# Optimization experiments

Measured on AMD Instinct MI355X. Metric: run time of the kernel, lower is better.

## Reference

```python
import jax, jax.numpy as jnp
import numpy as np

HIDDEN_DIM = 64
MEMORY_SLOTS = 4
SEQ_LEN = 24
VOCAB_SIZE = 64
B = 65536


def setup_inputs() -> dict:
    key = jax.random.key(0)
    ks = jax.random.split(key, 16)
    s = 0.05
    inp = {
        "seqs": jax.random.randint(ks[0], (B, SEQ_LEN), 0, VOCAB_SIZE + 2),
        "query_tok": jax.random.randint(ks[1], (B,), 0, VOCAB_SIZE + 2),
        # embedding table [VOCAB+2, H]
        "embed": jax.random.normal(ks[2], (VOCAB_SIZE + 2, HIDDEN_DIM), jnp.float32) * s,
        # joint_net: Linear(H + S*H -> H), ReLU, Linear(H -> H), ReLU  (weights stored [in, out])
        "W1": jax.random.normal(ks[3], (HIDDEN_DIM + MEMORY_SLOTS * HIDDEN_DIM, HIDDEN_DIM), jnp.float32) * s,
        "b1": jax.random.normal(ks[4], (HIDDEN_DIM,), jnp.float32) * s,
        "W2": jax.random.normal(ks[5], (HIDDEN_DIM, HIDDEN_DIM), jnp.float32) * s,
        "b2": jax.random.normal(ks[6], (HIDDEN_DIM,), jnp.float32) * s,
        # write_head: Linear(H -> H)
        "Ww": jax.random.normal(ks[7], (HIDDEN_DIM, HIDDEN_DIM), jnp.float32) * s,
        "bw": jax.random.normal(ks[8], (HIDDEN_DIM,), jnp.float32) * s,
        # evict_head: Linear(H -> MEMORY_SLOTS)
        "We": jax.random.normal(ks[9], (HIDDEN_DIM, MEMORY_SLOTS), jnp.float32) * s,
        "be": jax.random.normal(ks[10], (MEMORY_SLOTS,), jnp.float32) * s,
        # read_head: Linear(2H -> H), ReLU, Linear(H -> VOCAB)
        "Wr1": jax.random.normal(ks[11], (2 * HIDDEN_DIM, HIDDEN_DIM), jnp.float32) * s,
        "br1": jax.random.normal(ks[12], (HIDDEN_DIM,), jnp.float32) * s,
        "Wr2": jax.random.normal(ks[13], (HIDDEN_DIM, VOCAB_SIZE), jnp.float32) * s,
        "br2": jax.random.normal(ks[14], (VOCAB_SIZE,), jnp.float32) * s,
    }
    return inp


def reference(seqs, query_tok, embed, W1, b1, W2, b2, Ww, bw, We, be, Wr1, br1, Wr2, br2):
    # Token embeddings for the first SEQ_LEN-1 positions, scanned over time: [T, B, H]
    emb_seq = jnp.swapaxes(embed[seqs[:, : SEQ_LEN - 1]], 0, 1)

    def step(mem, emb_t):  # mem: [B, S, H], emb_t: [B, H]
        joint_in = jnp.concatenate([emb_t, mem.reshape(mem.shape[0], -1)], axis=-1)  # [B, H + S*H]
        h = jax.nn.relu(joint_in @ W1 + b1)
        h = jax.nn.relu(h @ W2 + b2)                      # [B, H]
        write_vec = h @ Ww + bw                           # [B, H]
        evict_logits = h @ We + be                        # [B, S]
        evict_idx = jnp.argmax(evict_logits, axis=-1)     # [B] hard, non-diff
        mask = jax.nn.one_hot(evict_idx, MEMORY_SLOTS, dtype=bool)[..., None]  # [B, S, 1]
        new_mem = jnp.where(mask, write_vec[:, None, :], mem)
        return new_mem, None

    mem0 = jnp.zeros((seqs.shape[0], MEMORY_SLOTS, HIDDEN_DIM), jnp.float32)
    mem, _ = jax.lax.scan(step, mem0, emb_seq)

    mem_summary = mem.mean(axis=1)                        # [B, H]
    q_emb = embed[query_tok]                              # [B, H]
    r = jnp.concatenate([q_emb, mem_summary], axis=-1)    # [B, 2H]
    logits = jax.nn.relu(r @ Wr1 + br1) @ Wr2 + br2       # [B, VOCAB]
    return logits
```

## Files before the change

### kernel.cpp

```cpp
#include <hip/hip_runtime.h>

#define H       64
#define NSLOT   4
#define NSTEP   23
#define NB      65536
#define NV      66
#define SEQL    24
#define LPE     8
#define GELEM   2
#define TPB     512
#define EPB     128
#define ACTSTR  132
#define W1RSTR  68
#define W1SSTR  (64 * W1RSTR + 8)

#define OFF_EW1   0
#define OFF_EWR1  (NV * H)

__global__ __launch_bounds__(256) void k_setup_tables(
    const float* __restrict__ embed, const float* __restrict__ W1, const float* __restrict__ b1,
    const float* __restrict__ Wr1, const float* __restrict__ br1, float* __restrict__ ws)
{
    int idx = blockIdx.x * 256 + threadIdx.x;
    if (idx >= NV * H) return;
    int t = idx >> 6, k = idx & 63;
    float a1 = b1[k], a2 = br1[k];
    for (int j = 0; j < H; ++j) {
        float e = embed[t * H + j];
        a1 = fmaf(e, W1[j * H + k], a1);
        a2 = fmaf(e, Wr1[j * H + k], a2);
    }
    ws[OFF_EW1 + idx]  = a1;
    ws[OFF_EWR1 + idx] = a2;
}

#define FMA8V(w0, w1, a, ACC) do {                                          \
    ACC[0]=fmaf((a),w0.x,ACC[0]); ACC[1]=fmaf((a),w0.y,ACC[1]);            \
    ACC[2]=fmaf((a),w0.z,ACC[2]); ACC[3]=fmaf((a),w0.w,ACC[3]);            \
    ACC[4]=fmaf((a),w1.x,ACC[4]); ACC[5]=fmaf((a),w1.y,ACC[5]);            \
    ACC[6]=fmaf((a),w1.z,ACC[6]); ACC[7]=fmaf((a),w1.w,ACC[7]);            \
} while (0)

#define LOAD8(ptr, A) do {                                                  \
    const float4* _b = (const float4*)(ptr);                                \
    float4 _b0 = _b[0], _b1 = _b[1];                                        \
    A[0]=_b0.x; A[1]=_b0.y; A[2]=_b0.z; A[3]=_b0.w;                        \
    A[4]=_b1.x; A[5]=_b1.y; A[6]=_b1.z; A[7]=_b1.w;                        \
} while (0)

__global__ __launch_bounds__(TPB, 2) void k_main(
    const float* __restrict__ W1, const float* __restrict__ W2, const float* __restrict__ b2,
    const float* __restrict__ Ww, const float* __restrict__ bw,
    const float* __restrict__ We, const float* __restrict__ be,
    const float* __restrict__ Wr1, const float* __restrict__ Wr2, const float* __restrict__ br2,
    const int* __restrict__ qtok, const int* __restrict__ seqs,
    const float* __restrict__ ws, float* __restrict__ out)
{
    __shared__ float sW1m[NSLOT * W1SSTR];
    __shared__ float act[H * ACTSTR];
    __shared__ float sWe[H * NSLOT];

    const int tid  = threadIdx.x;
    const int m    = tid & (LPE - 1);
    const int g    = tid >> 3;
    const int eA   = g;
    const int eB   = g + 64;
    const int gidA = blockIdx.x * EPB + eA;
    const int gidB = blockIdx.x * EPB + eB;
    const int k0   = m * 8;
    const int slot = m & 3;

    for (int i = tid; i < NSLOT * H * H; i += TPB) {
        int s = i >> 12, r = (i >> 6) & 63, k = i & 63;
        sW1m[s * W1SSTR + r * W1RSTR + k] = W1[(H + s * H + r) * H + k];
    }
    if (tid < H * NSLOT) sWe[tid] = We[tid];
    __syncthreads();

    const float* embW1b  = ws + OFF_EW1;
    const float* embWr1b = ws + OFF_EWR1;

    float mA0[8], mA1[8], mA2[8], mA3[8], cA[8];
    float mB0[8], mB1[8], mB2[8], mB3[8], cB[8];
#pragma unroll
    for (int i = 0; i < 8; ++i) {
        mA0[i]=0.f; mA1[i]=0.f; mA2[i]=0.f; mA3[i]=0.f; cA[i]=0.f;
        mB0[i]=0.f; mB1[i]=0.f; mB2[i]=0.f; mB3[i]=0.f; cB[i]=0.f;
    }

    float b2r[8], bwr[8];
    LOAD8(b2 + k0, b2r);
    LOAD8(bw + k0, bwr);
    const float bes = be[slot];

    int tokA = seqs[gidA * SEQL];
    int tokB = seqs[gidB * SEQL];

    float accA[8], accB[8];

#pragma unroll 1
    for (int t = 0; t < NSTEP; ++t) {
        int tokAn = seqs[gidA * SEQL + t + 1];
        int tokBn = seqs[gidB * SEQL + t + 1];

        {
            float hA[8], hB[8];
            LOAD8(embW1b + tokA * H + k0, hA);
            LOAD8(embW1b + tokB * H + k0, hB);
#pragma unroll
            for (int i = 0; i < 8; ++i) {
                act[(k0 + i) * ACTSTR + eA] = fmaxf(hA[i] + cA[i], 0.f);
                act[(k0 + i) * ACTSTR + eB] = fmaxf(hB[i] + cB[i], 0.f);
            }
        }

#pragma unroll
        for (int i = 0; i < 8; ++i) { accA[i] = b2r[i]; accB[i] = b2r[i]; }
#pragma unroll 4
        for (int j = 0; j < H; ++j) {
            const float4* w = (const float4*)(W2 + j * H + k0);
            float4 w0 = w[0], w1 = w[1];
            float a0 = act[j * ACTSTR + eA];
            float a1 = act[j * ACTSTR + eB];
            FMA8V(w0, w1, a0, accA);
            FMA8V(w0, w1, a1, accB);
        }
#pragma unroll
        for (int i = 0; i < 8; ++i) {
            act[(k0 + i) * ACTSTR + eA] = fmaxf(accA[i], 0.f);
            act[(k0 + i) * ACTSTR + eB] = fmaxf(accB[i], 0.f);
        }

        float lgA = bes, lgB = bes;
#pragma unroll
        for (int i = 0; i < 8; ++i) { accA[i] = bwr[i]; accB[i] = bwr[i]; }
#pragma unroll 4
        for (int j = 0; j < H; ++j) {
            const float4* w = (const float4*)(Ww + j * H + k0);
            float4 w0 = w[0], w1 = w[1];
            float a0 = act[j * ACTSTR + eA];
            float a1 = act[j * ACTSTR + eB];
            FMA8V(w0, w1, a0, accA);
            FMA8V(w0, w1, a1, accB);
            float we = sWe[j * NSLOT + slot];
            lgA = fmaf(a0, we, lgA);
            lgB = fmaf(a1, we, lgB);
        }

        int base = (tid & 63) & ~(LPE - 1);
        float vA0 = __shfl(lgA, base + 0), vA1 = __shfl(lgA, base + 1);
        float vA2 = __shfl(lgA, base + 2), vA3 = __shfl(lgA, base + 3);
        float vB0 = __shfl(lgB, base + 0), vB1 = __shfl(lgB, base + 1);
        float vB2 = __shfl(lgB, base + 2), vB3 = __shfl(lgB, base + 3);
        int eSA = 0; float bstA = vA0;
        if (vA1 > bstA) { bstA = vA1; eSA = 1; }
        if (vA2 > bstA) { bstA = vA2; eSA = 2; }
        if (vA3 > bstA) { bstA = vA3; eSA = 3; }
        int eSB = 0; float bstB = vB0;
        if (vB1 > bstB) { bstB = vB1; eSB = 1; }
        if (vB2 > bstB) { bstB = vB2; eSB = 2; }
        if (vB3 > bstB) { bstB = vB3; eSB = 3; }

        {
            bool a0 = (eSA == 0), a1 = (eSA == 1), a2 = (eSA == 2), a3 = (eSA == 3);
            bool b0 = (eSB == 0), b1 = (eSB == 1), b2_ = (eSB == 2), b3 = (eSB == 3);
#pragma unroll
            for (int i = 0; i < 8; ++i) {
                float oldA = a0 ? mA0[i] : a1 ? mA1[i] : a2 ? mA2[i] : mA3[i];
                float oldB = b0 ? mB0[i] : b1 ? mB1[i] : b2_ ? mB2[i] : mB3[i];
                float wA = accA[i], wB = accB[i];
                mA0[i] = a0 ? wA : mA0[i];  mA1[i] = a1 ? wA : mA1[i];
                mA2[i] = a2 ? wA : mA2[i];  mA3[i] = a3 ? wA : mA3[i];
                mB0[i] = b0 ? wB : mB0[i];  mB1[i] = b1 ? wB : mB1[i];
                mB2[i] = b2_ ? wB : mB2[i]; mB3[i] = b3 ? wB : mB3[i];
                act[(k0 + i) * ACTSTR + eA] = wA - oldA;
                act[(k0 + i) * ACTSTR + eB] = wB - oldB;
            }
        }

        const float* WA = sW1m + eSA * W1SSTR + k0;
        const float* WB = sW1m + eSB * W1SSTR + k0;
#pragma unroll 4
        for (int j = 0; j < H; ++j) {
            const float4* wa = (const float4*)(WA + j * W1RSTR);
            const float4* wb = (const float4*)(WB + j * W1RSTR);
            float4 wa0 = wa[0], wa1 = wa[1];
            float4 wb0 = wb[0], wb1 = wb[1];
            float dA = act[j * ACTSTR + eA];
            float dB = act[j * ACTSTR + eB];
            FMA8V(wa0, wa1, dA, cA);
            FMA8V(wb0, wb1, dB, cB);
        }

        tokA = tokAn; tokB = tokBn;
    }

#pragma unroll
    for (int i = 0; i < 8; ++i) {
        act[(k0 + i) * ACTSTR + eA] = 0.25f * (mA0[i] + mA1[i] + mA2[i] + mA3[i]);
        act[(k0 + i) * ACTSTR + eB] = 0.25f * (mB0[i] + mB1[i] + mB2[i] + mB3[i]);
    }

    int qA = qtok[gidA], qB = qtok[gidB];
    LOAD8(embWr1b + qA * H + k0, accA);
    LOAD8(embWr1b + qB * H + k0, accB);
#pragma unroll 4
    for (int j = 0; j < H; ++j) {
        const float4* w = (const float4*)(Wr1 + (H + j) * H + k0);
        float4 w0 = w[0], w1 = w[1];
        float a0 = act[j * ACTSTR + eA];
        float a1 = act[j * ACTSTR + eB];
        FMA8V(w0, w1, a0, accA);
        FMA8V(w0, w1, a1, accB);
    }
#pragma unroll
    for (int i = 0; i < 8; ++i) {
        act[(k0 + i) * ACTSTR + eA] = fmaxf(accA[i], 0.f);
        act[(k0 + i) * ACTSTR + eB] = fmaxf(accB[i], 0.f);
    }

    LOAD8(br2 + k0, accA);
#pragma unroll
    for (int i = 0; i < 8; ++i) accB[i] = accA[i];
#pragma unroll 4
    for (int j = 0; j < H; ++j) {
        const float4* w = (const float4*)(Wr2 + j * H + k0);
        float4 w0 = w[0], w1 = w[1];
        float a0 = act[j * ACTSTR + eA];
        float a1 = act[j * ACTSTR + eB];
        FMA8V(w0, w1, a0, accA);
        FMA8V(w0, w1, a1, accB);
    }

    float4* oA = (float4*)(out + (size_t)gidA * H + k0);
    oA[0] = make_float4(accA[0], accA[1], accA[2], accA[3]);
    oA[1] = make_float4(accA[4], accA[5], accA[6], accA[7]);
    float4* oB = (float4*)(out + (size_t)gidB * H + k0);
    oB[0] = make_float4(accB[0], accB[1], accB[2], accB[3]);
    oB[1] = make_float4(accB[4], accB[5], accB[6], accB[7]);
}

extern "C" void kernel_launch(void* const* d_in, const int* in_sizes, int n_in,
                              void* d_out, int out_size, void* d_ws, size_t ws_size,
                              hipStream_t stream)
{
    const int*   seqs  = (const int*)d_in[0];
    const int*   qtok  = (const int*)d_in[1];
    const float* embed = (const float*)d_in[2];
    const float* W1    = (const float*)d_in[3];
    const float* b1    = (const float*)d_in[4];
    const float* W2    = (const float*)d_in[5];
    const float* b2    = (const float*)d_in[6];
    const float* Ww    = (const float*)d_in[7];
    const float* bw    = (const float*)d_in[8];
    const float* We    = (const float*)d_in[9];
    const float* be    = (const float*)d_in[10];
    const float* Wr1   = (const float*)d_in[11];
    const float* br1   = (const float*)d_in[12];
    const float* Wr2   = (const float*)d_in[13];
    const float* br2   = (const float*)d_in[14];
    float* out = (float*)d_out;
    float* ws  = (float*)d_ws;

    hipLaunchKernelGGL(k_setup_tables, dim3((NV * H + 255) / 256), dim3(256), 0, stream,
                       embed, W1, b1, Wr1, br1, ws);
    hipLaunchKernelGGL(k_main, dim3(NB / EPB), dim3(TPB), 0, stream,
                       W1, W2, b2, Ww, bw, We, be, Wr1, Wr2, br2, qtok, seqs, ws, out);
}
```

Measured before the change: 932.5 us.

## Transpose activation tile to per-element rows and stage W2/Ww in LDS

The shared activation buffer changes from a feature-major layout to one row per batch element, so each lane reads activations as float4 vectors instead of scalars. W2 and Ww are now copied into shared memory rather than read from global memory on every step. The W1 memory-slot weights are split: only the first three lanes' column blocks are kept in LDS and the rest come from global memory. This frees LDS for the new buffers, but it adds a lane-divergent branch inside the inner loop and may cause bank conflicts on the per-row writes.

```diff
diff --git a/kernel.cpp b/kernel.cpp
--- a/kernel.cpp
+++ b/kernel.cpp
@@ -7,12 +7,12 @@
 #define NV      66
 #define SEQL    24
 #define LPE     8
-#define GELEM   2
 #define TPB     512
 #define EPB     128
-#define ACTSTR  132
-#define W1RSTR  68
-#define W1SSTR  (64 * W1RSTR + 8)
+#define ACTSTR  68
+#define KLM     3
+#define W1LROW  24
+#define W1LSLOT 1540
 
 #define OFF_EW1   0
 #define OFF_EWR1  (NV * H)
@@ -56,9 +56,11 @@
     const int* __restrict__ qtok, const int* __restrict__ seqs,
     const float* __restrict__ ws, float* __restrict__ out)
 {
-    __shared__ float sW1m[NSLOT * W1SSTR];
-    __shared__ float act[H * ACTSTR];
-    __shared__ float sWe[H * NSLOT];
+    __shared__ float sW2[H * H];
+    __shared__ float sWw[H * H];
+    __shared__ float sW1m[NSLOT * W1LSLOT];
+    __shared__ float sAct[EPB * ACTSTR];
+    __shared__ float sWeT[NSLOT * H];
 
     const int tid  = threadIdx.x;
     const int m    = tid & (LPE - 1);
@@ -70,11 +72,20 @@
     const int k0   = m * 8;
     const int slot = m & 3;
 
-    for (int i = tid; i < NSLOT * H * H; i += TPB) {
-        int s = i >> 12, r = (i >> 6) & 63, k = i & 63;
-        sW1m[s * W1SSTR + r * W1RSTR + k] = W1[(H + s * H + r) * H + k];
-    }
-    if (tid < H * NSLOT) sWe[tid] = We[tid];
+    for (int i = tid; i < H * H; i += TPB) { sW2[i] = W2[i]; sWw[i] = Ww[i]; }
+    if (tid < NSLOT * H * H / 16) {
+    }
+    if (tid < 256) {
+        int s = tid >> 6, j = tid & 63;
+        const float* src = W1 + (H + s * H + j) * H;
+        float* dst = sW1m + s * W1LSLOT + j * W1LROW;
+#pragma unroll
+        for (int k = 0; k < KLM * 8; ++k) dst[k] = src[k];
+    }
+    if (tid < NSLOT * H) {
+        int j = tid >> 2, s = tid & 3;
+        sWeT[s * H + j] = We[j * NSLOT + s];
+    }
     __syncthreads();
 
     const float* embW1b  = ws + OFF_EW1;
@@ -97,6 +108,8 @@
     int tokB = seqs[gidB * SEQL];
 
     float accA[8], accB[8];
+    float* rowA = sAct + eA * ACTSTR;
+    float* rowB = sAct + eB * ACTSTR;
 
 #pragma unroll 1
     for (int t = 0; t < NSTEP; ++t) {
@@ -109,42 +122,53 @@
             LOAD8(embW1b + tokB * H + k0, hB);
 #pragma unroll
             for (int i = 0; i < 8; ++i) {
-                act[(k0 + i) * ACTSTR + eA] = fmaxf(hA[i] + cA[i], 0.f);
-                act[(k0 + i) * ACTSTR + eB] = fmaxf(hB[i] + cB[i], 0.f);
+                rowA[k0 + i] = fmaxf(hA[i] + cA[i], 0.f);
+                rowB[k0 + i] = fmaxf(hB[i] + cB[i], 0.f);
             }
         }
 
 #pragma unroll
         for (int i = 0; i < 8; ++i) { accA[i] = b2r[i]; accB[i] = b2r[i]; }
 #pragma unroll 4
-        for (int j = 0; j < H; ++j) {
-            const float4* w = (const float4*)(W2 + j * H + k0);
-            float4 w0 = w[0], w1 = w[1];
-            float a0 = act[j * ACTSTR + eA];
-            float a1 = act[j * ACTSTR + eB];
-            FMA8V(w0, w1, a0, accA);
-            FMA8V(w0, w1, a1, accB);
+        for (int jq = 0; jq < 16; ++jq) {
+            float4 a4 = *(const float4*)(rowA + jq * 4);
+            float4 b4 = *(const float4*)(rowB + jq * 4);
+            float aAv[4] = {a4.x, a4.y, a4.z, a4.w};
+            float aBv[4] = {b4.x, b4.y, b4.z, b4.w};
+#pragma unroll
+            for (int jj = 0; jj < 4; ++jj) {
+                const float4* w = (const float4*)(sW2 + (jq * 4 + jj) * H + k0);
+                float4 w0 = w[0], w1 = w[1];
+                FMA8V(w0, w1, aAv[jj], accA);
+                FMA8V(w0, w1, aBv[jj], accB);
+            }
         }
 #pragma unroll
         for (int i = 0; i < 8; ++i) {
-            act[(k0 + i) * ACTSTR + eA] = fmaxf(accA[i], 0.f);
-            act[(k0 + i) * ACTSTR + eB] = fmaxf(accB[i], 0.f);
+            rowA[k0 + i] = fmaxf(accA[i], 0.f);
+            rowB[k0 + i] = fmaxf(accB[i], 0.f);
         }
 
         float lgA = bes, lgB = bes;
 #pragma unroll
         for (int i = 0; i < 8; ++i) { accA[i] = bwr[i]; accB[i] = bwr[i]; }
 #pragma unroll 4
-        for (int j = 0; j < H; ++j) {
-            const float4* w = (const float4*)(Ww + j * H + k0);
-            float4 w0 = w[0], w1 = w[1];
-            float a0 = act[j * ACTSTR + eA];
-            float a1 = act[j * ACTSTR + eB];
-            FMA8V(w0, w1, a0, accA);
-            FMA8V(w0, w1, a1, accB);
-            float we = sWe[j * NSLOT + slot];
-            lgA = fmaf(a0, we, lgA);
-            lgB = fmaf(a1, we, lgB);
+        for (int jq = 0; jq < 16; ++jq) {
+            float4 a4 = *(const float4*)(rowA + jq * 4);
+            float4 b4 = *(const float4*)(rowB + jq * 4);
+            float4 we4 = *(const float4*)(sWeT + slot * H + jq * 4);
+            float aAv[4] = {a4.x, a4.y, a4.z, a4.w};
+            float aBv[4] = {b4.x, b4.y, b4.z, b4.w};
+            float wev[4] = {we4.x, we4.y, we4.z, we4.w};
+#pragma unroll
+            for (int jj = 0; jj < 4; ++jj) {
+                const float4* w = (const float4*)(sWw + (jq * 4 + jj) * H + k0);
+                float4 w0 = w[0], w1 = w[1];
+                FMA8V(w0, w1, aAv[jj], accA);
+                FMA8V(w0, w1, aBv[jj], accB);
+                lgA = fmaf(aAv[jj], wev[jj], lgA);
+                lgB = fmaf(aBv[jj], wev[jj], lgB);
+            }
         }
 
         int base = (tid & 63) & ~(LPE - 1);
@@ -173,23 +197,39 @@
                 mA2[i] = a2 ? wA : mA2[i];  mA3[i] = a3 ? wA : mA3[i];
                 mB0[i] = b0 ? wB : mB0[i];  mB1[i] = b1 ? wB : mB1[i];
                 mB2[i] = b2_ ? wB : mB2[i]; mB3[i] = b3 ? wB : mB3[i];
-                act[(k0 + i) * ACTSTR + eA] = wA - oldA;
-                act[(k0 + i) * ACTSTR + eB] = wB - oldB;
-            }
-        }
-
-        const float* WA = sW1m + eSA * W1SSTR + k0;
-        const float* WB = sW1m + eSB * W1SSTR + k0;
-#pragma unroll 4
-        for (int j = 0; j < H; ++j) {
-            const float4* wa = (const float4*)(WA + j * W1RSTR);
-            const float4* wb = (const float4*)(WB + j * W1RSTR);
-            float4 wa0 = wa[0], wa1 = wa[1];
-            float4 wb0 = wb[0], wb1 = wb[1];
-            float dA = act[j * ACTSTR + eA];
-            float dB = act[j * ACTSTR + eB];
-            FMA8V(wa0, wa1, dA, cA);
-            FMA8V(wb0, wb1, dB, cB);
+                rowA[k0 + i] = wA - oldA;
+                rowB[k0 + i] = wB - oldB;
+            }
+        }
+
+        const float* lA = sW1m + eSA * W1LSLOT + k0;
+        const float* lB = sW1m + eSB * W1LSLOT + k0;
+        const float* gA = W1 + (size_t)(H + eSA * H) * H + k0;
+        const float* gB = W1 + (size_t)(H + eSB * H) * H + k0;
+#pragma unroll 4
+        for (int jq = 0; jq < 16; ++jq) {
+            float4 a4 = *(const float4*)(rowA + jq * 4);
+            float4 b4 = *(const float4*)(rowB + jq * 4);
+            float dAv[4] = {a4.x, a4.y, a4.z, a4.w};
+            float dBv[4] = {b4.x, b4.y, b4.z, b4.w};
+#pragma unroll
+            for (int jj = 0; jj < 4; ++jj) {
+                int j = jq * 4 + jj;
+                float4 w0A, w1A, w0B, w1B;
+                if (m < KLM) {
+                    const float4* wa = (const float4*)(lA + j * W1LROW);
+                    const float4* wb = (const float4*)(lB + j * W1LROW);
+                    w0A = wa[0]; w1A = wa[1];
+                    w0B = wb[0]; w1B = wb[1];
+                } else {
+                    const float4* wa = (const float4*)(gA + j * H);
+                    const float4* wb = (const float4*)(gB + j * H);
+                    w0A = wa[0]; w1A = wa[1];
+                    w0B = wb[0]; w1B = wb[1];
+                }
+                FMA8V(w0A, w1A, dAv[jj], cA);
+                FMA8V(w0B, w1B, dBv[jj], cB);
+            }
         }
 
         tokA = tokAn; tokB = tokBn;
@@ -197,39 +237,49 @@
 
 #pragma unroll
     for (int i = 0; i < 8; ++i) {
-        act[(k0 + i) * ACTSTR + eA] = 0.25f * (mA0[i] + mA1[i] + mA2[i] + mA3[i]);
-        act[(k0 + i) * ACTSTR + eB] = 0.25f * (mB0[i] + mB1[i] + mB2[i] + mB3[i]);
+        rowA[k0 + i] = 0.25f * (mA0[i] + mA1[i] + mA2[i] + mA3[i]);
+        rowB[k0 + i] = 0.25f * (mB0[i] + mB1[i] + mB2[i] + mB3[i]);
     }
 
     int qA = qtok[gidA], qB = qtok[gidB];
     LOAD8(embWr1b + qA * H + k0, accA);
     LOAD8(embWr1b + qB * H + k0, accB);
 #pragma unroll 4
-    for (int j = 0; j < H; ++j) {
-        const float4* w = (const float4*)(Wr1 + (H + j) * H + k0);
-        float4 w0 = w[0], w1 = w[1];
-        float a0 = act[j * ACTSTR + eA];
-        float a1 = act[j * ACTSTR + eB];
-        FMA8V(w0, w1, a0, accA);
-        FMA8V(w0, w1, a1, accB);
+    for (int jq = 0; jq < 16; ++jq) {
+        float4 a4 = *(const float4*)(rowA + jq * 4);
+        float4 b4 = *(const float4*)(rowB + jq * 4);
+        float aAv[4] = {a4.x, a4.y, a4.z, a4.w};
+        float aBv[4] = {b4.x, b4.y, b4.z, b4.w};
+#pragma unroll
+        for (int jj = 0; jj < 4; ++jj) {
+            const float4* w = (const float4*)(Wr1 + (H + jq * 4 + jj) * H + k0);
+            float4 w0 = w[0], w1 = w[1];
+            FMA8V(w0, w1, aAv[jj], accA);
+            FMA8V(w0, w1, aBv[jj], accB);
+        }
     }
 #pragma unroll
     for (int i = 0; i < 8; ++i) {
-        act[(k0 + i) * ACTSTR + eA] = fmaxf(accA[i], 0.f);
-        act[(k0 + i) * ACTSTR + eB] = fmaxf(accB[i], 0.f);
+        rowA[k0 + i] = fmaxf(accA[i], 0.f);
+        rowB[k0 + i] = fmaxf(accB[i], 0.f);
     }
 
     LOAD8(br2 + k0, accA);
 #pragma unroll
     for (int i = 0; i < 8; ++i) accB[i] = accA[i];
 #pragma unroll 4
-    for (int j = 0; j < H; ++j) {
-        const float4* w = (const float4*)(Wr2 + j * H + k0);
-        float4 w0 = w[0], w1 = w[1];
-        float a0 = act[j * ACTSTR + eA];
-        float a1 = act[j * ACTSTR + eB];
-        FMA8V(w0, w1, a0, accA);
-        FMA8V(w0, w1, a1, accB);
+    for (int jq = 0; jq < 16; ++jq) {
+        float4 a4 = *(const float4*)(rowA + jq * 4);
+        float4 b4 = *(const float4*)(rowB + jq * 4);
+        float aAv[4] = {a4.x, a4.y, a4.z, a4.w};
+        float aBv[4] = {b4.x, b4.y, b4.z, b4.w};
+#pragma unroll
+        for (int jj = 0; jj < 4; ++jj) {
+            const float4* w = (const float4*)(Wr2 + (jq * 4 + jj) * H + k0);
+            float4 w0 = w[0], w1 = w[1];
+            FMA8V(w0, w1, aAv[jj], accA);
+            FMA8V(w0, w1, aBv[jj], accB);
+        }
     }
 
     float4* oA = (float4*)(out + (size_t)gidA * H + k0);
```

New measurement: 2.958 ms. +217.2%, slower.
